# Kernel optimization log

Hardware: AMD Instinct MI355X
Metric: run time of the kernel (lower is better)

## Reference

```python
import jax, jax.numpy as jnp
import numpy as np

B, T, D = 4, 8192, 1024

def setup_inputs() -> dict:
    key = jax.random.key(0)
    k1, k2, k3 = jax.random.split(key, 3)
    x = jax.random.normal(k1, (B, T, D), dtype=jnp.float32)
    decay = jax.random.normal(k2, (D,), dtype=jnp.float32)
    freq = jax.random.normal(k3, (D,), dtype=jnp.float32)
    return {"x": x, "decay": decay, "freq": freq}

def reference(x, decay, freq):
    Bb, Tt, Dd = x.shape
    t = jnp.arange(Tt, dtype=jnp.float32)  # [T]
    # kernel: [T, D]
    k = jnp.exp(-jnp.abs(decay)[None, :] * t[:, None]) * jnp.cos(freq[None, :] * t[:, None])
    n_fft = 2 * Tt
    x_f = jnp.fft.rfft(x.astype(jnp.float32), n=n_fft, axis=1)   # [B, T+1, D] complex
    k_f = jnp.fft.rfft(k, n=n_fft, axis=0)                        # [T+1, D] complex
    y = jnp.fft.irfft(x_f * k_f[None, :, :], n=n_fft, axis=1)    # [B, 2T, D]
    return y[:, :Tt, :].astype(x.dtype)
```

## Files before the change

kernel.cpp:

```cpp
#include <hip/hip_runtime.h>
#include <cmath>

#define BB 4
#define TT 8192
#define DD 1024
#define DBLK 16
#define NDB (DD/DBLK)
#define NCHAIN (BB*NDB)
#define CL 1024
#define NITER (TT/CL)
#define NTHR 512
#define NPART (NTHR/DBLK)
#define PLEN (CL/NPART)


__global__ __launch_bounds__(NTHR, 2) void fftconv_persist(
    const float* __restrict__ x, const float* __restrict__ decay,
    const float* __restrict__ freq, float* __restrict__ y)
{
    __shared__ float  tile[2][CL*DBLK];
    __shared__ float2 Ssub[NPART][DBLK];
    __shared__ float2 eoff[NPART][DBLK];
    __shared__ float2 HB[DBLK];

    const int tid  = threadIdx.x;
    const int l16  = tid & 15;
    const int part = tid >> 4;
    const int wv   = tid >> 6;
    const int wl   = tid & 63;
    const int bid  = blockIdx.x;
    const int chain = (bid & 7)*32 + (bid >> 3);
    const int dblk  = chain & (NDB-1);
    const int b     = chain >> 6;
    const int d     = dblk*DBLK + l16;

    const float a = fabsf(decay[d]);
    const float w = freq[d];
    float s_, c_, e;
    e = expf(-a);                    sincosf(w, &s_, &c_);
    const float rr = e*c_, ri = e*s_;
    e = expf(-a*(float)PLEN);        sincosf(w*(float)PLEN, &s_, &c_);
    const float Msr = e*c_, Msi = e*s_;
    e = expf(-a*(float)CL);          sincosf(w*(float)CL, &s_, &c_);
    const float Mcr = e*c_, Mci = e*s_;
    e = expf(-a*(float)(PLEN*part)); sincosf(w*(float)(PLEN*part), &s_, &c_);
    const float Mpr = e*c_, Mpi = e*s_;

    const float* xch = x + (size_t)b*TT*DD + dblk*DBLK;
    float*       ych = y + (size_t)b*TT*DD + dblk*DBLK;

    auto stage = [&](int k, int buf) {
        const float* xc = xch + (size_t)(k*CL)*DD;
#pragma unroll
        for (int i = 0; i < 8; ++i) {
            const int u0 = (wv*8 + i)*64;
            const int up = u0 + wl;
            const int ul = up ^ (((up >> 7) & 1) << 2);
            __builtin_amdgcn_global_load_lds(
                (const __attribute__((address_space(1))) void*)
                    (xc + (size_t)(ul >> 2)*DD + ((ul & 3) << 2)),
                (__attribute__((address_space(3))) void*)&tile[buf][u0 << 2],
                16, 0, 0);
        }
    };

    float Hr = 0.f, Hi = 0.f;
    const int cxor = (part & 1) << 4;

    stage(0, 0);

    for (int k = 0; k < NITER; ++k) {
        const int cur = k & 1;

        if (k + 1 < NITER) stage(k + 1, cur ^ 1);

        if (k == 0)                asm volatile("s_waitcnt vmcnt(8)"  ::: "memory");
        else if (k + 1 < NITER)    asm volatile("s_waitcnt vmcnt(40)" ::: "memory");
        else                       asm volatile("s_waitcnt vmcnt(32)" ::: "memory");
        __builtin_amdgcn_s_barrier();
        __builtin_amdgcn_sched_barrier(0);

        float hRr[PLEN];
        {
            float hr = 0.f, hi = 0.f;
            const int fbase = part << 9;
#pragma unroll
            for (int t = 0; t < PLEN; ++t) {
                float xv = tile[cur][(fbase + (t << 4) + l16) ^ cxor];
                float nr = fmaf(rr, hr, fmaf(-ri, hi, xv));
                hi = fmaf(rr, hi, ri*hr);
                hr = nr;
                hRr[t] = hr;
            }
            Ssub[part][l16] = make_float2(hr, hi);
        }
        asm volatile("s_waitcnt lgkmcnt(0)" ::: "memory");
        __builtin_amdgcn_s_barrier();
        __builtin_amdgcn_sched_barrier(0);

        if (tid < DBLK) {
            float Lr = 0.f, Li = 0.f;
#pragma unroll
            for (int p = 0; p < NPART; ++p) {
                eoff[p][l16] = make_float2(Lr, Li);
                float2 Sp = Ssub[p][l16];
                float nr = fmaf(Msr, Lr, fmaf(-Msi, Li, Sp.x));
                Li = fmaf(Msr, Li, fmaf(Msi, Lr, Sp.y));
                Lr = nr;
            }
            HB[l16] = make_float2(Hr, Hi);
            float nHr = fmaf(Mcr, Hr, fmaf(-Mci, Hi, Lr));
            Hi = fmaf(Mcr, Hi, fmaf(Mci, Hr, Li));
            Hr = nHr;
        }
        asm volatile("s_waitcnt lgkmcnt(0)" ::: "memory");
        __builtin_amdgcn_s_barrier();
        __builtin_amdgcn_sched_barrier(0);

        {
            float2 Hp = HB[l16];
            float2 eo = eoff[part][l16];
            float Sr = eo.x + (Mpr*Hp.x - Mpi*Hp.y);
            float Si = eo.y + (Mpr*Hp.y + Mpi*Hp.x);
            float wr = rr*Sr - ri*Si;
            float wi = rr*Si + ri*Sr;
            float* yp = ych + (size_t)(k*CL + part*PLEN)*DD + l16;
#pragma unroll
            for (int t = 0; t < PLEN; ++t) {
                yp[(size_t)t*DD] = hRr[t] + wr;
                float nwr = rr*wr - ri*wi;
                wi = rr*wi + ri*wr;
                wr = nwr;
            }
        }
    }
}

extern "C" void kernel_launch(void* const* d_in, const int* in_sizes, int n_in,
                              void* d_out, int out_size, void* d_ws, size_t ws_size,
                              hipStream_t stream) {
    const float* x     = (const float*)d_in[0];
    const float* decay = (const float*)d_in[1];
    const float* freq  = (const float*)d_in[2];
    float*       y     = (float*)d_out;

    fftconv_persist<<<NCHAIN, NTHR, 0, stream>>>(x, decay, freq, y);
}
```

Before: 51.75 us.

## Double block size and split carry scan into two-level grouped scan

Raises threads per block from 512 to 1024, halving each thread's sequential sub-chunk length (PLEN 32 to 16) and halving the loads each thread stages. The cross-partition carry scan, now over 64 partitions, becomes two levels: 8 groups of 8 partitions are scanned in parallel, then 16 threads scan the 8 group sums including the chunk carry. This shortens the serial recurrence per thread and the serial scan length, at the cost of one extra barrier per chunk and occupancy dropping to one block per CU.

```diff
diff --git a/kernel.cpp b/kernel.cpp
--- a/kernel.cpp
+++ b/kernel.cpp
@@ -9,19 +9,21 @@
 #define NCHAIN (BB*NDB)
 #define CL 1024
 #define NITER (TT/CL)
-#define NTHR 512
+#define NTHR 1024
 #define NPART (NTHR/DBLK)
 #define PLEN (CL/NPART)
+#define NGRP 8
 
 
-__global__ __launch_bounds__(NTHR, 2) void fftconv_persist(
+__global__ __launch_bounds__(NTHR, 1) void fftconv_persist(
     const float* __restrict__ x, const float* __restrict__ decay,
     const float* __restrict__ freq, float* __restrict__ y)
 {
     __shared__ float  tile[2][CL*DBLK];
     __shared__ float2 Ssub[NPART][DBLK];
     __shared__ float2 eoff[NPART][DBLK];
-    __shared__ float2 HB[DBLK];
+    __shared__ float2 Gs[NGRP][DBLK];
+    __shared__ float2 Eg[NGRP][DBLK];
 
     const int tid  = threadIdx.x;
     const int l16  = tid & 15;
@@ -37,14 +39,17 @@
     const float a = fabsf(decay[d]);
     const float w = freq[d];
     float s_, c_, e;
-    e = expf(-a);                    sincosf(w, &s_, &c_);
+    e = expf(-a);                     sincosf(w, &s_, &c_);
     const float rr = e*c_, ri = e*s_;
-    e = expf(-a*(float)PLEN);        sincosf(w*(float)PLEN, &s_, &c_);
+    e = expf(-a*(float)PLEN);         sincosf(w*(float)PLEN, &s_, &c_);
     const float Msr = e*c_, Msi = e*s_;
-    e = expf(-a*(float)CL);          sincosf(w*(float)CL, &s_, &c_);
-    const float Mcr = e*c_, Mci = e*s_;
-    e = expf(-a*(float)(PLEN*part)); sincosf(w*(float)(PLEN*part), &s_, &c_);
-    const float Mpr = e*c_, Mpi = e*s_;
+    e = expf(-a*(float)(PLEN*NGRP));  sincosf(w*(float)(PLEN*NGRP), &s_, &c_);
+    const float Mgr = e*c_, Mgi = e*s_;
+    {
+        const float tj = (float)(PLEN*(part & (NGRP-1)));
+        e = expf(-a*tj); sincosf(w*tj, &s_, &c_);
+    }
+    const float Mjr = e*c_, Mji = e*s_;
 
     const float* xch = x + (size_t)b*TT*DD + dblk*DBLK;
     float*       ych = y + (size_t)b*TT*DD + dblk*DBLK;
@@ -52,10 +57,10 @@
     auto stage = [&](int k, int buf) {
         const float* xc = xch + (size_t)(k*CL)*DD;
 #pragma unroll
-        for (int i = 0; i < 8; ++i) {
-            const int u0 = (wv*8 + i)*64;
+        for (int i = 0; i < 4; ++i) {
+            const int u0 = (wv*4 + i)*64;
             const int up = u0 + wl;
-            const int ul = up ^ (((up >> 7) & 1) << 2);
+            const int ul = up ^ (((up >> 6) & 1) << 2);
             __builtin_amdgcn_global_load_lds(
                 (const __attribute__((address_space(1))) void*)
                     (xc + (size_t)(ul >> 2)*DD + ((ul & 3) << 2)),
@@ -74,16 +79,16 @@
 
         if (k + 1 < NITER) stage(k + 1, cur ^ 1);
 
-        if (k == 0)                asm volatile("s_waitcnt vmcnt(8)"  ::: "memory");
-        else if (k + 1 < NITER)    asm volatile("s_waitcnt vmcnt(40)" ::: "memory");
-        else                       asm volatile("s_waitcnt vmcnt(32)" ::: "memory");
+        if (k == 0)             asm volatile("s_waitcnt vmcnt(4)"  ::: "memory");
+        else if (k + 1 < NITER) asm volatile("s_waitcnt vmcnt(20)" ::: "memory");
+        else                    asm volatile("s_waitcnt vmcnt(16)" ::: "memory");
         __builtin_amdgcn_s_barrier();
         __builtin_amdgcn_sched_barrier(0);
 
         float hRr[PLEN];
         {
             float hr = 0.f, hi = 0.f;
-            const int fbase = part << 9;
+            const int fbase = part << 8;
 #pragma unroll
             for (int t = 0; t < PLEN; ++t) {
                 float xv = tile[cur][(fbase + (t << 4) + l16) ^ cxor];
@@ -98,30 +103,47 @@
         __builtin_amdgcn_s_barrier();
         __builtin_amdgcn_sched_barrier(0);
 
+        if (tid < NGRP*DBLK) {
+            const int sp = tid >> 4;
+            const int l  = tid & 15;
+            float Wr = 0.f, Wi = 0.f;
+#pragma unroll
+            for (int j = 0; j < NGRP; ++j) {
+                const int p = sp*NGRP + j;
+                eoff[p][l] = make_float2(Wr, Wi);
+                float2 Sp = Ssub[p][l];
+                float nr = fmaf(Msr, Wr, fmaf(-Msi, Wi, Sp.x));
+                Wi = fmaf(Msr, Wi, fmaf(Msi, Wr, Sp.y));
+                Wr = nr;
+            }
+            Gs[sp][l] = make_float2(Wr, Wi);
+        }
+        asm volatile("s_waitcnt lgkmcnt(0)" ::: "memory");
+        __builtin_amdgcn_s_barrier();
+        __builtin_amdgcn_sched_barrier(0);
+
         if (tid < DBLK) {
-            float Lr = 0.f, Li = 0.f;
+            float Er = Hr, Ei = Hi;
 #pragma unroll
-            for (int p = 0; p < NPART; ++p) {
-                eoff[p][l16] = make_float2(Lr, Li);
-                float2 Sp = Ssub[p][l16];
-                float nr = fmaf(Msr, Lr, fmaf(-Msi, Li, Sp.x));
-                Li = fmaf(Msr, Li, fmaf(Msi, Lr, Sp.y));
-                Lr = nr;
+            for (int g = 0; g < NGRP; ++g) {
+                Eg[g][l16] = make_float2(Er, Ei);
+                float2 G = Gs[g][l16];
+                float nr = fmaf(Mgr, Er, fmaf(-Mgi, Ei, G.x));
+                Ei = fmaf(Mgr, Ei, fmaf(Mgi, Er, G.y));
+                Er = nr;
             }
-            HB[l16] = make_float2(Hr, Hi);
-            float nHr = fmaf(Mcr, Hr, fmaf(-Mci, Hi, Lr));
-            Hi = fmaf(Mcr, Hi, fmaf(Mci, Hr, Li));
-            Hr = nHr;
+            Hr = Er; Hi = Ei;
         }
         asm volatile("s_waitcnt lgkmcnt(0)" ::: "memory");
         __builtin_amdgcn_s_barrier();
         __builtin_amdgcn_sched_barrier(0);
 
         {
-            float2 Hp = HB[l16];
+            const int g = part >> 3;
             float2 eo = eoff[part][l16];
-            float Sr = eo.x + (Mpr*Hp.x - Mpi*Hp.y);
-            float Si = eo.y + (Mpr*Hp.y + Mpi*Hp.x);
+            float2 Ev = Eg[g][l16];
+            float Sr = eo.x + (Mjr*Ev.x - Mji*Ev.y);
+            float Si = eo.y + (Mjr*Ev.y + Mji*Ev.x);
             float wr = rr*Sr - ri*Si;
             float wi = rr*Si + ri*Sr;
             float* yp = ych + (size_t)(k*CL + part*PLEN)*DD + l16;
```

Measured after the change: 50.83 us. Within noise of the previous version (-1.8%).
